# Optimization experiments

Hardware: AMD Instinct MI355X
Metric: run time of the kernel (lower is better)

The kernel has to match this reference:

```python
import jax, jax.numpy as jnp
import numpy as np

DIM = 512
NUM_HEADS = 8
HEAD_DIM = DIM // NUM_HEADS
SCALE = HEAD_DIM ** -0.5


def setup_inputs() -> dict:
    key = jax.random.key(0)
    k1, k2, k3, k4 = jax.random.split(key, 4)
    x = jax.random.normal(k1, (2, 4096, DIM), dtype=jnp.float32)
    # Linear weights stored as (in, out) for x @ W; torch Linear(dim, 3*dim, bias=False)
    w_qkv = jax.random.normal(k2, (DIM, 3 * DIM), dtype=jnp.float32) * (DIM ** -0.5)
    w_proj = jax.random.normal(k3, (DIM, DIM), dtype=jnp.float32) * (DIM ** -0.5)
    b_proj = jax.random.normal(k4, (DIM,), dtype=jnp.float32) * 0.02
    return {"x": x, "w_qkv": w_qkv, "w_proj": w_proj, "b_proj": b_proj}


def reference(x, w_qkv, w_proj, b_proj):
    B, N, C = x.shape
    qkv = (x @ w_qkv).reshape(B, N, 3, NUM_HEADS, HEAD_DIM)
    qkv = jnp.transpose(qkv, (2, 0, 3, 1, 4))  # (3, B, H, N, hd)
    q, k, v = qkv[0], qkv[1], qkv[2]
    attn = jnp.einsum("bhnd,bhmd->bhnm", q, k) * SCALE
    attn = jax.nn.softmax(attn, axis=-1)
    out = jnp.einsum("bhnm,bhmd->bhnd", attn, v)
    out = jnp.transpose(out, (0, 2, 1, 3)).reshape(B, N, C)
    return out @ w_proj + b_proj
```

## Files before the change

### kernel.cpp

```cpp
#include <hip/hip_runtime.h>
#include <hip/hip_bf16.h>
#include <stdint.h>
#include <math.h>

#define NC3 1536
#define QSCALE 0.18033688011111907f

typedef __attribute__((ext_vector_type(8))) short short8;
typedef __attribute__((ext_vector_type(4))) short short4v;
typedef __attribute__((ext_vector_type(4))) float f32x4;

static __device__ __forceinline__ short f2bf(float f) {
    union { __hip_bfloat16 h; short s; } u;
    u.h = __float2bfloat16(f);
    return u.s;
}
static __device__ __forceinline__ unsigned bfpack(float a, float b) {
    unsigned ua = (__float_as_uint(a) + 0x8000u) >> 16;
    unsigned ub = (__float_as_uint(b) + 0x8000u) & 0xffff0000u;
    return ua | ub;
}

#define GLD_LDS(g, l)                                                          \
    __builtin_amdgcn_global_load_lds(                                          \
        (const __attribute__((address_space(1))) void*)(g),                    \
        (__attribute__((address_space(3))) void*)(l), 16, 0, 0)

__global__ __launch_bounds__(256) void cast_f32_bf16(const float* __restrict__ src,
                                                     short* __restrict__ dst, int n4) {
    int i = blockIdx.x * 256 + threadIdx.x;
    if (i < n4) {
        float4 v = ((const float4*)src)[i];
        short4v o = {f2bf(v.x), f2bf(v.y), f2bf(v.z), f2bf(v.w)};
        ((short4v*)dst)[i] = o;
    }
}

__global__ __launch_bounds__(256) void transpose_f32_bf16(const float* __restrict__ src,
                                                          short* __restrict__ dst,
                                                          int R, int C) {
    __shared__ short t[32][33];
    int c0 = blockIdx.x * 32, r0 = blockIdx.y * 32;
    int tx = threadIdx.x, ty = threadIdx.y;
#pragma unroll
    for (int i = 0; i < 4; i++)
        t[ty + i * 8][tx] = f2bf(src[(size_t)(r0 + ty + i * 8) * C + c0 + tx]);
    __syncthreads();
#pragma unroll
    for (int i = 0; i < 4; i++)
        dst[(size_t)(c0 + ty + i * 8) * R + r0 + tx] = t[tx][ty + i * 8];
}

__global__ __launch_bounds__(256) void transpose_v(const short* __restrict__ QKV,
                                                   short* __restrict__ VT) {
    __shared__ short t[32][33];
    int n0 = blockIdx.x * 32, d0 = blockIdx.y * 32;
    int bh = blockIdx.z;
    int b = bh >> 3, h = bh & 7;
    const short* src = QKV + (size_t)b * 4096 * NC3 + 1024 + h * 64;
    short* dst = VT + (size_t)bh * 64 * 4096;
    int tx = threadIdx.x, ty = threadIdx.y;
#pragma unroll
    for (int i = 0; i < 4; i++)
        t[ty + i * 8][tx] = src[(size_t)(n0 + ty + i * 8) * NC3 + d0 + tx];
    __syncthreads();
#pragma unroll
    for (int i = 0; i < 4; i++)
        dst[(size_t)(d0 + ty + i * 8) * 4096 + n0 + tx] = t[tx][ty + i * 8];
}

template <int NMODE>
__global__ __launch_bounds__(256) void gemm128(const short* __restrict__ A,
                                               const short* __restrict__ Bt,
                                               short* __restrict__ OutB,
                                               float* __restrict__ OutF,
                                               const float* __restrict__ bias) {
    __shared__ __attribute__((aligned(16))) short a_sm[128 * 64];
    __shared__ __attribute__((aligned(16))) short b_sm[128 * 64];
    const int tid = threadIdx.x;
    const int lane = tid & 63;
    const int wave = tid >> 6;
    const int wr = wave >> 1, wc = wave & 1;
    const int quad = lane >> 4;
    const int l15 = lane & 15;
    const int m0 = blockIdx.x * 128;
    const int n0 = blockIdx.y * 128;
    const int srow = lane >> 3;
    const int schunk = (lane & 7) ^ srow;

    f32x4 zero4 = {0.f, 0.f, 0.f, 0.f};
    f32x4 acc[4][4];
#pragma unroll
    for (int i = 0; i < 4; i++)
#pragma unroll
        for (int j = 0; j < 4; j++) acc[i][j] = zero4;

    for (int k0 = 0; k0 < 512; k0 += 64) {
        __syncthreads();
#pragma unroll
        for (int i = 0; i < 4; i++) {
            int r0 = wave * 32 + i * 8;
            const short* ga = A + (size_t)(m0 + r0 + srow) * 512 + k0 + schunk * 8;
            GLD_LDS(ga, a_sm + r0 * 64);
            const short* gb = Bt + (size_t)(n0 + r0 + srow) * 512 + k0 + schunk * 8;
            GLD_LDS(gb, b_sm + r0 * 64);
        }
        __syncthreads();
#pragma unroll
        for (int kk = 0; kk < 2; kk++) {
            short8 af[4], bfr[4];
#pragma unroll
            for (int mi = 0; mi < 4; mi++) {
                int row = wr * 64 + mi * 16 + l15;
                int slot = (kk * 4 + quad) ^ (row & 7);
                af[mi] = *(const short8*)(a_sm + row * 64 + slot * 8);
            }
#pragma unroll
            for (int ni = 0; ni < 4; ni++) {
                int row = wc * 64 + ni * 16 + l15;
                int slot = (kk * 4 + quad) ^ (row & 7);
                bfr[ni] = *(const short8*)(b_sm + row * 64 + slot * 8);
            }
#pragma unroll
            for (int mi = 0; mi < 4; mi++)
#pragma unroll
                for (int ni = 0; ni < 4; ni++)
                    acc[mi][ni] = __builtin_amdgcn_mfma_f32_16x16x32_bf16(
                        af[mi], bfr[ni], acc[mi][ni], 0, 0, 0);
        }
    }

#pragma unroll
    for (int mi = 0; mi < 4; mi++) {
#pragma unroll
        for (int ni = 0; ni < 4; ni++) {
            int gm0 = m0 + wr * 64 + mi * 16 + quad * 4;
            int gn = n0 + wc * 64 + ni * 16 + l15;
            f32x4 v = acc[mi][ni];
#pragma unroll
            for (int r = 0; r < 4; r++) {
                int gm = gm0 + r;
                float val = v[r];
                if (NMODE == 0) {
                    float o = (gn < 512) ? val * QSCALE : val;
                    OutB[(size_t)gm * NC3 + gn] = f2bf(o);
                } else {
                    OutF[(size_t)gm * 512 + gn] = val + bias[gn];
                }
            }
        }
    }
}

__global__ __launch_bounds__(256, 2) void attn_kernel(const short* __restrict__ QKV,
                                                      const short* __restrict__ VT,
                                                      short* __restrict__ AO) {
    __shared__ __attribute__((aligned(16))) short k_sm[2][64 * 64];
    __shared__ __attribute__((aligned(16))) short v_sm[2][64 * 64];
    __shared__ __attribute__((aligned(16))) short p_sm[128 * 64];

    const int tid = threadIdx.x;
    const int lane = tid & 63;
    const int wave = tid >> 6;
    const int quad = lane >> 4;
    const int l15 = lane & 15;
    const int l7 = l15 & 7;
    const int qt = blockIdx.x;
    const int bh = blockIdx.y;
    const int b = bh >> 3, h = bh & 7;
    const size_t tokbase = (size_t)b * 4096;
    const int rowbase = qt * 128;
    const short* Qg = QKV + h * 64;
    const short* Kg = QKV + 512 + h * 64;
    const short* VTg = VT + (size_t)bh * 64 * 4096;
    const int srow = lane >> 3;
    const int schunk = (lane & 7) ^ srow;

#pragma unroll
    for (int i = 0; i < 4; i++) {
        int r0 = wave * 32 + i * 8;
        GLD_LDS(Qg + (tokbase + rowbase + r0 + srow) * NC3 + schunk * 8, p_sm + r0 * 64);
    }
#pragma unroll
    for (int i = 0; i < 2; i++) {
        int r0 = wave * 16 + i * 8;
        GLD_LDS(Kg + (tokbase + r0 + srow) * NC3 + schunk * 8, k_sm[0] + r0 * 64);
        GLD_LDS(VTg + (size_t)(r0 + srow) * 4096 + schunk * 8, v_sm[0] + r0 * 64);
    }
    __syncthreads();

    short8 qf[2][2];
#pragma unroll
    for (int mi = 0; mi < 2; mi++)
#pragma unroll
        for (int kk = 0; kk < 2; kk++) {
            int row = wave * 32 + mi * 16 + l15;
            int slot = (kk * 4 + quad) ^ l7;
            qf[mi][kk] = *(const short8*)(p_sm + row * 64 + slot * 8);
        }

    const short onebf = (short)0x3F80;
    const short8 ones = {onebf, onebf, onebf, onebf, onebf, onebf, onebf, onebf};

    f32x4 zero4 = {0.f, 0.f, 0.f, 0.f};
    f32x4 acc_o[2][4];
    f32x4 acc_l[2];
#pragma unroll
    for (int mi = 0; mi < 2; mi++) {
        acc_l[mi] = zero4;
#pragma unroll
        for (int ni = 0; ni < 4; ni++) acc_o[mi][ni] = zero4;
    }

    for (int kt = 0; kt < 64; kt++) {
        __syncthreads();
        const int cur = kt & 1;
        if (kt < 63) {
            const int nb = cur ^ 1;
#pragma unroll
            for (int i = 0; i < 2; i++) {
                int r0 = wave * 16 + i * 8;
                GLD_LDS(Kg + (tokbase + (size_t)(kt + 1) * 64 + r0 + srow) * NC3 + schunk * 8,
                        k_sm[nb] + r0 * 64);
                GLD_LDS(VTg + (size_t)(r0 + srow) * 4096 + (kt + 1) * 64 + schunk * 8,
                        v_sm[nb] + r0 * 64);
            }
        }

        f32x4 s[2][4];
#pragma unroll
        for (int mi = 0; mi < 2; mi++)
#pragma unroll
            for (int ki = 0; ki < 4; ki++) s[mi][ki] = zero4;
#pragma unroll
        for (int kk = 0; kk < 2; kk++) {
#pragma unroll
            for (int ki = 0; ki < 4; ki++) {
                int row = ki * 16 + l15;
                int slot = (kk * 4 + quad) ^ l7;
                short8 kf = *(const short8*)(k_sm[cur] + row * 64 + slot * 8);
#pragma unroll
                for (int mi = 0; mi < 2; mi++)
                    s[mi][ki] = __builtin_amdgcn_mfma_f32_16x16x32_bf16(
                        kf, qf[mi][kk], s[mi][ki], 0, 0, 0);
            }
        }

#pragma unroll
        for (int mi = 0; mi < 2; mi++) {
            int prow = wave * 32 + mi * 16 + l15;
#pragma unroll
            for (int ki = 0; ki < 4; ki++) {
                float p0 = __builtin_amdgcn_exp2f(s[mi][ki][0]);
                float p1 = __builtin_amdgcn_exp2f(s[mi][ki][1]);
                float p2 = __builtin_amdgcn_exp2f(s[mi][ki][2]);
                float p3 = __builtin_amdgcn_exp2f(s[mi][ki][3]);
                uint2 pk;
                pk.x = bfpack(p0, p1);
                pk.y = bfpack(p2, p3);
                int u16 = ki * 2 + (quad >> 1);
                *(uint2*)(p_sm + prow * 64 + (u16 ^ l7) * 8 + (quad & 1) * 4) = pk;
            }
        }

#pragma unroll
        for (int mi = 0; mi < 2; mi++) {
            int prow = wave * 32 + mi * 16 + l15;
#pragma unroll
            for (int kk = 0; kk < 2; kk++) {
                short8 pf = *(const short8*)(p_sm + prow * 64 + ((kk * 4 + quad) ^ l7) * 8);
                acc_l[mi] = __builtin_amdgcn_mfma_f32_16x16x32_bf16(pf, ones, acc_l[mi], 0, 0, 0);
#pragma unroll
                for (int ni = 0; ni < 4; ni++) {
                    int row = ni * 16 + l15;
                    int slot = (kk * 4 + quad) ^ l7;
                    short8 vf = *(const short8*)(v_sm[cur] + row * 64 + slot * 8);
                    acc_o[mi][ni] = __builtin_amdgcn_mfma_f32_16x16x32_bf16(
                        pf, vf, acc_o[mi][ni], 0, 0, 0);
                }
            }
        }
    }

#pragma unroll
    for (int mi = 0; mi < 2; mi++) {
#pragma unroll
        for (int r = 0; r < 4; r++) {
            float inv = 1.0f / acc_l[mi][r];
            size_t grow = tokbase + rowbase + wave * 32 + mi * 16 + quad * 4 + r;
#pragma unroll
            for (int ni = 0; ni < 4; ni++) {
                int col = h * 64 + ni * 16 + l15;
                AO[grow * 512 + col] = f2bf(acc_o[mi][ni][r] * inv);
            }
        }
    }
}

extern "C" void kernel_launch(void* const* d_in, const int* in_sizes, int n_in,
                              void* d_out, int out_size, void* d_ws, size_t ws_size,
                              hipStream_t stream) {
    (void)in_sizes; (void)n_in; (void)out_size; (void)ws_size;
    const float* x = (const float*)d_in[0];
    const float* wqkv = (const float*)d_in[1];
    const float* wproj = (const float*)d_in[2];
    const float* bproj = (const float*)d_in[3];
    float* out = (float*)d_out;

    short* ws = (short*)d_ws;
    short* xbf = ws;
    short* wqkvT = xbf + (size_t)4194304;
    short* wprojT = wqkvT + (size_t)1536 * 512;
    short* QKV = wprojT + (size_t)512 * 512;
    short* VTb = QKV + (size_t)8192 * 1536;
    short* AO = VTb + (size_t)16 * 64 * 4096;

    cast_f32_bf16<<<4096, 256, 0, stream>>>(x, xbf, 1048576);
    transpose_f32_bf16<<<dim3(48, 16), dim3(32, 8), 0, stream>>>(wqkv, wqkvT, 512, 1536);
    transpose_f32_bf16<<<dim3(16, 16), dim3(32, 8), 0, stream>>>(wproj, wprojT, 512, 512);
    gemm128<0><<<dim3(64, 12), 256, 0, stream>>>(xbf, wqkvT, QKV, nullptr, nullptr);
    transpose_v<<<dim3(128, 2, 16), dim3(32, 8), 0, stream>>>(QKV, VTb);
    attn_kernel<<<dim3(32, 16), 256, 0, stream>>>(QKV, VTb, AO);
    gemm128<1><<<dim3(64, 4), 256, 0, stream>>>(AO, wprojT, nullptr, out, bproj);
}
```

Before: 210.2 us.

## Switch attention to 32x32x16 MFMA and keep P in registers via lane shuffles

The attention kernel now uses 32x32x16 bf16 MFMAs with transposed operand roles (K·Q^T and V·P^T), so each lane holds one query row. The softmax probabilities are repacked between MFMA output and input layouts with cross-half-wave shuffles, which removes the P round-trip through shared memory and its LDS buffer. The output goes through a swizzled LDS staging area and is written to global memory as 16-byte vector stores. This lowers LDS traffic and footprint, at the cost of extra shuffles and a larger accumulator register footprint that may affect occupancy.

```diff
diff --git a/kernel.cpp b/kernel.cpp
--- a/kernel.cpp
+++ b/kernel.cpp
@@ -9,6 +9,7 @@
 typedef __attribute__((ext_vector_type(8))) short short8;
 typedef __attribute__((ext_vector_type(4))) short short4v;
 typedef __attribute__((ext_vector_type(4))) float f32x4;
+typedef __attribute__((ext_vector_type(16))) float f32x16;
 
 static __device__ __forceinline__ short f2bf(float f) {
     union { __hip_bfloat16 h; short s; } u;
@@ -157,14 +158,12 @@
                                                       short* __restrict__ AO) {
     __shared__ __attribute__((aligned(16))) short k_sm[2][64 * 64];
     __shared__ __attribute__((aligned(16))) short v_sm[2][64 * 64];
-    __shared__ __attribute__((aligned(16))) short p_sm[128 * 64];
 
     const int tid = threadIdx.x;
     const int lane = tid & 63;
     const int wave = tid >> 6;
-    const int quad = lane >> 4;
-    const int l15 = lane & 15;
-    const int l7 = l15 & 7;
+    const int l31 = lane & 31;
+    const int hi = lane >> 5;
     const int qt = blockIdx.x;
     const int bh = blockIdx.y;
     const int b = bh >> 3, h = bh & 7;
@@ -176,41 +175,35 @@
     const int srow = lane >> 3;
     const int schunk = (lane & 7) ^ srow;
 
+    short* qstage = &k_sm[0][0];
 #pragma unroll
     for (int i = 0; i < 4; i++) {
         int r0 = wave * 32 + i * 8;
-        GLD_LDS(Qg + (tokbase + rowbase + r0 + srow) * NC3 + schunk * 8, p_sm + r0 * 64);
-    }
+        GLD_LDS(Qg + (tokbase + rowbase + r0 + srow) * NC3 + schunk * 8, qstage + r0 * 64);
+    }
+    __syncthreads();
+    const int qrow = wave * 32 + l31;
+    short8 qf[4];
+#pragma unroll
+    for (int kk = 0; kk < 4; kk++) {
+        int slot = (kk * 2 + hi) ^ (qrow & 7);
+        qf[kk] = *(const short8*)(qstage + qrow * 64 + slot * 8);
+    }
+    __syncthreads();
+
 #pragma unroll
     for (int i = 0; i < 2; i++) {
         int r0 = wave * 16 + i * 8;
         GLD_LDS(Kg + (tokbase + r0 + srow) * NC3 + schunk * 8, k_sm[0] + r0 * 64);
         GLD_LDS(VTg + (size_t)(r0 + srow) * 4096 + schunk * 8, v_sm[0] + r0 * 64);
     }
-    __syncthreads();
-
-    short8 qf[2][2];
-#pragma unroll
-    for (int mi = 0; mi < 2; mi++)
-#pragma unroll
-        for (int kk = 0; kk < 2; kk++) {
-            int row = wave * 32 + mi * 16 + l15;
-            int slot = (kk * 4 + quad) ^ l7;
-            qf[mi][kk] = *(const short8*)(p_sm + row * 64 + slot * 8);
-        }
 
     const short onebf = (short)0x3F80;
     const short8 ones = {onebf, onebf, onebf, onebf, onebf, onebf, onebf, onebf};
 
-    f32x4 zero4 = {0.f, 0.f, 0.f, 0.f};
-    f32x4 acc_o[2][4];
-    f32x4 acc_l[2];
-#pragma unroll
-    for (int mi = 0; mi < 2; mi++) {
-        acc_l[mi] = zero4;
-#pragma unroll
-        for (int ni = 0; ni < 4; ni++) acc_o[mi][ni] = zero4;
-    }
+    f32x16 acc_o[2], acc_l;
+#pragma unroll
+    for (int i = 0; i < 16; i++) { acc_o[0][i] = 0.f; acc_o[1][i] = 0.f; acc_l[i] = 0.f; }
 
     for (int kt = 0; kt < 64; kt++) {
         __syncthreads();
@@ -227,73 +220,83 @@
             }
         }
 
-        f32x4 s[2][4];
-#pragma unroll
-        for (int mi = 0; mi < 2; mi++)
-#pragma unroll
-            for (int ki = 0; ki < 4; ki++) s[mi][ki] = zero4;
-#pragma unroll
-        for (int kk = 0; kk < 2; kk++) {
-#pragma unroll
-            for (int ki = 0; ki < 4; ki++) {
-                int row = ki * 16 + l15;
-                int slot = (kk * 4 + quad) ^ l7;
+        f32x16 s[2];
+#pragma unroll
+        for (int i = 0; i < 16; i++) { s[0][i] = 0.f; s[1][i] = 0.f; }
+#pragma unroll
+        for (int kk = 0; kk < 4; kk++) {
+#pragma unroll
+            for (int kb = 0; kb < 2; kb++) {
+                int row = kb * 32 + l31;
+                int slot = (kk * 2 + hi) ^ (row & 7);
                 short8 kf = *(const short8*)(k_sm[cur] + row * 64 + slot * 8);
-#pragma unroll
-                for (int mi = 0; mi < 2; mi++)
-                    s[mi][ki] = __builtin_amdgcn_mfma_f32_16x16x32_bf16(
-                        kf, qf[mi][kk], s[mi][ki], 0, 0, 0);
-            }
-        }
-
-#pragma unroll
-        for (int mi = 0; mi < 2; mi++) {
-            int prow = wave * 32 + mi * 16 + l15;
-#pragma unroll
-            for (int ki = 0; ki < 4; ki++) {
-                float p0 = __builtin_amdgcn_exp2f(s[mi][ki][0]);
-                float p1 = __builtin_amdgcn_exp2f(s[mi][ki][1]);
-                float p2 = __builtin_amdgcn_exp2f(s[mi][ki][2]);
-                float p3 = __builtin_amdgcn_exp2f(s[mi][ki][3]);
-                uint2 pk;
-                pk.x = bfpack(p0, p1);
-                pk.y = bfpack(p2, p3);
-                int u16 = ki * 2 + (quad >> 1);
-                *(uint2*)(p_sm + prow * 64 + (u16 ^ l7) * 8 + (quad & 1) * 4) = pk;
-            }
-        }
-
-#pragma unroll
-        for (int mi = 0; mi < 2; mi++) {
-            int prow = wave * 32 + mi * 16 + l15;
-#pragma unroll
-            for (int kk = 0; kk < 2; kk++) {
-                short8 pf = *(const short8*)(p_sm + prow * 64 + ((kk * 4 + quad) ^ l7) * 8);
-                acc_l[mi] = __builtin_amdgcn_mfma_f32_16x16x32_bf16(pf, ones, acc_l[mi], 0, 0, 0);
-#pragma unroll
-                for (int ni = 0; ni < 4; ni++) {
-                    int row = ni * 16 + l15;
-                    int slot = (kk * 4 + quad) ^ l7;
-                    short8 vf = *(const short8*)(v_sm[cur] + row * 64 + slot * 8);
-                    acc_o[mi][ni] = __builtin_amdgcn_mfma_f32_16x16x32_bf16(
-                        pf, vf, acc_o[mi][ni], 0, 0, 0);
-                }
-            }
-        }
-    }
-
-#pragma unroll
-    for (int mi = 0; mi < 2; mi++) {
-#pragma unroll
-        for (int r = 0; r < 4; r++) {
-            float inv = 1.0f / acc_l[mi][r];
-            size_t grow = tokbase + rowbase + wave * 32 + mi * 16 + quad * 4 + r;
-#pragma unroll
-            for (int ni = 0; ni < 4; ni++) {
-                int col = h * 64 + ni * 16 + l15;
-                AO[grow * 512 + col] = f2bf(acc_o[mi][ni][r] * inv);
-            }
-        }
+                s[kb] = __builtin_amdgcn_mfma_f32_32x32x16_bf16(kf, qf[kk], s[kb], 0, 0, 0);
+            }
+        }
+
+        unsigned pk[2][8];
+#pragma unroll
+        for (int kb = 0; kb < 2; kb++)
+#pragma unroll
+            for (int i = 0; i < 16; i += 2)
+                pk[kb][i >> 1] = bfpack(__builtin_amdgcn_exp2f(s[kb][i]),
+                                        __builtin_amdgcn_exp2f(s[kb][i + 1]));
+
+        short8 pf[4];
+#pragma unroll
+        for (int kb = 0; kb < 2; kb++) {
+#pragma unroll
+            for (int f = 0; f < 2; f++) {
+                unsigned b0 = pk[kb][4 * f + 0], b1 = pk[kb][4 * f + 1];
+                unsigned b2 = pk[kb][4 * f + 2], b3 = pk[kb][4 * f + 3];
+                unsigned s0 = hi ? b0 : b2;
+                unsigned s1 = hi ? b1 : b3;
+                unsigned t0 = (unsigned)__shfl_xor((int)s0, 32, 64);
+                unsigned t1 = (unsigned)__shfl_xor((int)s1, 32, 64);
+                union { unsigned u[4]; short8 s8; } cv;
+                cv.u[0] = hi ? t0 : b0;
+                cv.u[1] = hi ? t1 : b1;
+                cv.u[2] = hi ? b2 : t0;
+                cv.u[3] = hi ? b3 : t1;
+                pf[kb * 2 + f] = cv.s8;
+            }
+        }
+
+#pragma unroll
+        for (int g = 0; g < 4; g++) {
+            acc_l = __builtin_amdgcn_mfma_f32_32x32x16_bf16(ones, pf[g], acc_l, 0, 0, 0);
+#pragma unroll
+            for (int db = 0; db < 2; db++) {
+                int row = db * 32 + l31;
+                int slot = (g * 2 + hi) ^ (row & 7);
+                short8 vf = *(const short8*)(v_sm[cur] + row * 64 + slot * 8);
+                acc_o[db] = __builtin_amdgcn_mfma_f32_32x32x16_bf16(vf, pf[g], acc_o[db], 0, 0, 0);
+            }
+        }
+    }
+
+    __syncthreads();
+
+    float inv = 1.0f / acc_l[0];
+    short* osm = &k_sm[0][0] + wave * 2048;
+#pragma unroll
+    for (int db = 0; db < 2; db++) {
+#pragma unroll
+        for (int i = 0; i < 16; i += 2) {
+            int d = db * 32 + (i & 3) + 8 * (i >> 2) + 4 * hi;
+            unsigned pkd = bfpack(acc_o[db][i] * inv, acc_o[db][i + 1] * inv);
+            int slot = (d >> 3) ^ (l31 & 7);
+            *(unsigned*)(osm + l31 * 64 + slot * 8 + (d & 7)) = pkd;
+        }
+    }
+#pragma unroll
+    for (int j = 0; j < 4; j++) {
+        int r = lane >> 1;
+        int c = (lane & 1) * 4 + j;
+        int slot = c ^ (r & 7);
+        short8 ov = *(const short8*)(osm + r * 64 + slot * 8);
+        size_t grow = tokbase + rowbase + wave * 32 + r;
+        *(short8*)(AO + grow * 512 + h * 64 + c * 8) = ov;
     }
 }
 
```

Result: slower. 225.8 us (+7.4%).
